# Optimization experiments

Hardware: AMD Instinct MI355X
Metric: run time of the kernel (lower is better)

Reference implementation:

```python
import jax, jax.numpy as jnp
import numpy as np

K = 16  # hard-coded neighborhood size
EPS = 1e-5


def knn_idx(coor_k, coor_q, k):
    # coor_*: (B, 3, N). Returns idx (B, Nq, k) of k nearest points in coor_k for each query.
    inner = jnp.einsum('bcn,bcm->bnm', coor_q, coor_k)
    sq_q = jnp.sum(coor_q ** 2, axis=1)  # (B, Nq)
    sq_k = jnp.sum(coor_k ** 2, axis=1)  # (B, Nk)
    dist = sq_q[:, :, None] + sq_k[:, None, :] - 2.0 * inner  # (B, Nq, Nk)
    return jax.lax.top_k(-dist, k)[1]


def fps(coor, num_group):
    # furthest point sampling, matching pointnet2 (start at index 0, squared dists).
    B, _, N = coor.shape
    xyz = jnp.transpose(coor, (0, 2, 1))  # (B, N, 3)

    def step(carry, _):
        dist, last = carry
        centroid = jnp.take_along_axis(xyz, last[:, None, None], axis=1)  # (B,1,3)
        d = jnp.sum((xyz - centroid) ** 2, axis=-1)  # (B, N)
        dist = jnp.minimum(dist, d)
        nxt = jnp.argmax(dist, axis=1).astype(jnp.int32)
        return (dist, nxt), last

    init = (jnp.full((B, N), 1e10, dtype=coor.dtype), jnp.zeros((B,), jnp.int32))
    _, idxs = jax.lax.scan(step, init, None, length=num_group)
    return jnp.transpose(idxs, (1, 0))  # (B, num_group)


def gather_points(x, idx):
    # x: (B, C, N), idx: (B, S) -> (B, C, S)
    return jnp.take_along_axis(x, idx[:, None, :], axis=2)


def get_graph_feature(coor_q, x_q, coor_k, x_k):
    # coor: (B,3,N), x: (B,C,N) -> (B, 2C, Nq, K)
    B, C, Nq = x_q.shape
    idx = jax.lax.stop_gradient(knn_idx(coor_k, coor_q, K))  # (B, Nq, K)
    idx_flat = jnp.broadcast_to(idx.reshape(B, 1, Nq * K), (B, C, Nq * K))
    nbr = jnp.take_along_axis(x_k, idx_flat, axis=2).reshape(B, C, Nq, K)
    xq = x_q[..., None]  # (B, C, Nq, 1)
    return jnp.concatenate([nbr - xq, jnp.broadcast_to(xq, nbr.shape)], axis=1)


def group_norm(x, gamma, beta, groups):
    # x: (B, C, N, K); normalize over (C//G, N, K) per sample per group.
    B, C = x.shape[0], x.shape[1]
    xr = x.reshape(B, groups, C // groups, *x.shape[2:])
    red = tuple(range(2, xr.ndim))
    mean = jnp.mean(xr, axis=red, keepdims=True)
    var = jnp.mean((xr - mean) ** 2, axis=red, keepdims=True)
    xn = ((xr - mean) * jax.lax.rsqrt(var + EPS)).reshape(x.shape)
    shp = (1, C) + (1,) * (x.ndim - 2)
    return xn * gamma.reshape(shp) + beta.reshape(shp)


def lrelu(x):
    return jnp.where(x >= 0, x, 0.2 * x)


def edge_layer(f, w, g, b):
    # 1x1 conv (no bias) + GroupNorm(4) + LeakyReLU(0.2)
    f = jnp.einsum('oc,bcnk->bonk', w, f)
    return lrelu(group_norm(f, g, b, 4))


def setup_inputs() -> dict:
    key = jax.random.key(0)
    ks = jax.random.split(key, 16)
    B, N = 32, 2048
    p = {}
    p['x'] = jax.random.normal(ks[0], (B, 3, N), dtype=jnp.float32)
    p['w_in'] = jax.random.normal(ks[1], (8, 3), dtype=jnp.float32) * 0.3
    p['b_in'] = jax.random.normal(ks[2], (8,), dtype=jnp.float32) * 0.1
    dims = [(32, 16), (64, 64), (64, 128), (128, 128)]
    for i, (o, c) in enumerate(dims, start=1):
        kw, kg, kb = jax.random.split(ks[2 + i], 3)
        p[f'w{i}'] = jax.random.normal(kw, (o, c), dtype=jnp.float32) * (1.0 / np.sqrt(c))
        p[f'g{i}'] = 1.0 + 0.1 * jax.random.normal(kg, (o,), dtype=jnp.float32)
        p[f'b{i}'] = 0.1 * jax.random.normal(kb, (o,), dtype=jnp.float32)
    return p


def reference(x, w_in, b_in, w1, g1, b1, w2, g2, b2, w3, g3, b3, w4, g4, b4):
    coor = x
    f = jnp.einsum('oc,bcn->bon', w_in, x) + b_in[None, :, None]  # (B,8,N)

    f = get_graph_feature(coor, f, coor, f)          # (B,16,N,K)
    f = jnp.max(edge_layer(f, w1, g1, b1), axis=-1)  # (B,32,N)

    idx = jax.lax.stop_gradient(fps(coor, 512))
    coor_q, f_q = gather_points(coor, idx), gather_points(f, idx)
    f = get_graph_feature(coor_q, f_q, coor, f)      # (B,64,512,K)
    f = jnp.max(edge_layer(f, w2, g2, b2), axis=-1)  # (B,64,512)
    coor = coor_q

    f = get_graph_feature(coor, f, coor, f)          # (B,128,512,K)
    f = jnp.max(edge_layer(f, w3, g3, b3), axis=-1)  # (B,64,512)

    idx = jax.lax.stop_gradient(fps(coor, 128))
    coor_q, f_q = gather_points(coor, idx), gather_points(f, idx)
    f = get_graph_feature(coor_q, f_q, coor, f)      # (B,128,128,K)
    f = jnp.max(edge_layer(f, w4, g4, b4), axis=-1)  # (B,128,128)
    coor = coor_q
    return coor, f
```

## Files before the change

### kernel.cpp

```cpp
#include <hip/hip_runtime.h>
#include <hip/hip_bf16.h>

#define DEV __device__ __forceinline__
typedef unsigned long long u64;

DEV float bf2f(unsigned short u){ return __uint_as_float(((unsigned)u)<<16); }
DEV unsigned short f2bf(float f){
  unsigned u = __float_as_uint(f);
  u += 0x7fffu + ((u>>16)&1u);
  return (unsigned short)(u>>16);
}

template<int CTRL>
DEV u64 dpp_umax(u64 k){
  int lo = (int)(unsigned)k;
  int hi = (int)(unsigned)(k>>32);
  int plo = __builtin_amdgcn_update_dpp(lo, lo, CTRL, 0xF, 0xF, false);
  int phi = __builtin_amdgcn_update_dpp(hi, hi, CTRL, 0xF, 0xF, false);
  u64 p = ((u64)(unsigned)phi << 32) | (unsigned)plo;
  return (p > k) ? p : k;
}

DEV void ce64(u64 &a, u64 &b){
  u64 lo = (a<b)?a:b;
  u64 hi = (a<b)?b:a;
  a = lo; b = hi;
}
DEV void sort8(u64* x){
  #pragma unroll
  for (int k=2;k<=8;k<<=1){
    #pragma unroll
    for (int j=k>>1;j>0;j>>=1){
      #pragma unroll
      for (int i=0;i<8;++i){
        int l = i^j;
        if (l>i){
          if ((i&k)==0) ce64(x[i],x[l]);
          else          ce64(x[l],x[i]);
        }
      }
    }
  }
}
DEV void bm16(u64* A){
  #pragma unroll
  for (int gap=8;gap>0;gap>>=1){
    #pragma unroll
    for (int i=0;i<16;++i){
      if ((i&gap)==0) ce64(A[i], A[i|gap]);
    }
  }
}
DEV unsigned f2sort(float d){
  unsigned ub = __float_as_uint(d);
  unsigned s  = (unsigned)((int)ub >> 31);
  return ub ^ (s | 0x80000000u);
}

struct PConv {
  const void* s[14];
  float*      d[14];
  int         sz[14];
};

__global__ __launch_bounds__(256) void prep_kernel(
    const void* __restrict__ xraw, int* __restrict__ flagw,
    const void* __restrict__ w_in_raw, const void* __restrict__ b_in_raw,
    PConv p,
    float* __restrict__ xyz0, float* __restrict__ f0, float* __restrict__ stats){
  __shared__ int cnt;
  int t = threadIdx.x;
  if (t==0) cnt = 0;
  __syncthreads();
  {
    const unsigned short* xs = (const unsigned short*)xraw;
    int local = 0;
    for (int i=t; i<4096; i+=256){
      int e = (xs[i]>>7)&0xFF;
      if (e >= 0xC0) local++;
    }
    atomicAdd(&cnt, local);
  }
  __syncthreads();
  bool isf = (cnt > 64);
  int bx = blockIdx.x;
  if (bx==0 && t==0) *flagw = isf ? 1 : 0;
  if (bx < 117){
    int i = bx*256 + t;
    int seg = 0, off = i;
    #pragma unroll
    for (seg=0; seg<14; ++seg){
      if (off < p.sz[seg]) break;
      off -= p.sz[seg];
    }
    if (seg >= 14) return;
    float v = isf ? ((const float*)p.s[seg])[off]
                  : bf2f(((const unsigned short*)p.s[seg])[off]);
    p.d[seg][off] = v;
    return;
  }
  int i = (bx-117)*256 + t;
  if (i < 8192) stats[i] = 0.f;
  int b = i >> 11, n = i & 2047;
  size_t base = (size_t)b*3*2048 + n;
  float X, Y, Z;
  if (isf){
    const float* xf = (const float*)xraw;
    X = xf[base]; Y = xf[base+2048]; Z = xf[base+4096];
  } else {
    const unsigned short* xu = (const unsigned short*)xraw;
    X = bf2f(xu[base]); Y = bf2f(xu[base+2048]); Z = bf2f(xu[base+4096]);
  }
  float* o3 = xyz0 + (size_t)i*3;
  o3[0]=X; o3[1]=Y; o3[2]=Z;
  const float* wf = (const float*)w_in_raw;
  const float* bf = (const float*)b_in_raw;
  const unsigned short* wu = (const unsigned short*)w_in_raw;
  const unsigned short* bu = (const unsigned short*)b_in_raw;
  float* fo = f0 + (size_t)i*8;
  #pragma unroll
  for (int o=0;o<8;++o){
    float w0 = isf ? wf[o*3+0] : bf2f(wu[o*3+0]);
    float w1 = isf ? wf[o*3+1] : bf2f(wu[o*3+1]);
    float w2 = isf ? wf[o*3+2] : bf2f(wu[o*3+2]);
    float bb = isf ? bf[o]     : bf2f(bu[o]);
    fo[o] = w0*X + w1*Y + w2*Z + bb;
  }
}

template<int NK, int QB>
DEV void knn_body(float* smem, const float* __restrict__ qxyz,
                  const float* __restrict__ kxyz, int Nq,
                  int* __restrict__ oidx, int bx, int b){
  float4* kd = (float4*)smem;
  u64* lbuf  = (u64*)smem;
  int t = threadIdx.x;
  for (int i=t; i<NK; i+=256){
    const float* p = kxyz + ((size_t)b*NK + i)*3;
    float X=p[0], Y=p[1], Z=p[2];
    float sk = __fadd_rn(__fadd_rn(__fmul_rn(X,X),__fmul_rn(Y,Y)),__fmul_rn(Z,Z));
    kd[i] = make_float4(X,Y,Z,sk);
  }
  __syncthreads();
  int ql = t>>2, h = t&3;
  int q0 = bx*QB;
  const float* qp = qxyz + ((size_t)b*Nq + q0 + ql)*3;
  float QX=qp[0], QY=qp[1], QZ=qp[2];
  float sq = __fadd_rn(__fadd_rn(__fmul_rn(QX,QX),__fmul_rn(QY,QY)),__fmul_rn(QZ,QZ));
  u64 A[16];
  #pragma unroll
  for (int j=0;j<16;++j) A[j] = ~0ULL;
  #pragma unroll 1
  for (int i=0; i<NK/4; i+=8){
    u64 k8[8];
    #pragma unroll
    for (int u=0;u<8;++u){
      int cidx = 4*(i+u)+h;
      float4 c = kd[cidx];
      float dot = __fadd_rn(__fadd_rn(__fmul_rn(QX,c.x),__fmul_rn(QY,c.y)),__fmul_rn(QZ,c.z));
      float d = __fsub_rn(__fadd_rn(sq, c.w), __fmul_rn(2.0f,dot));
      k8[u] = ((u64)f2sort(d)<<32) | (unsigned)cidx;
    }
    sort8(k8);
    #pragma unroll
    for (int s=0;s<8;++s){
      u64 bb = k8[7-s];
      u64 a  = A[8+s];
      A[8+s] = (bb < a) ? bb : a;
    }
    bm16(A);
  }
  __syncthreads();
  u64* Lq = lbuf + ((size_t)ql*65 + (size_t)h*16);
  #pragma unroll
  for (int j=0;j<16;++j) Lq[j] = A[j];
  __syncthreads();
  if (t < QB){
    const u64* db = lbuf + (size_t)t*65;
    int p0=0,p1=0,p2=0,p3=0;
    u64 e0=db[0], e1=db[16], e2=db[32], e3=db[48];
    int* op = oidx + ((size_t)b*Nq + q0 + t)*16;
    #pragma unroll 1
    for (int j=0;j<16;++j){
      u64 bd = e0; int bh = 0;
      if (e1 < bd){ bd=e1; bh=1; }
      if (e2 < bd){ bd=e2; bh=2; }
      if (e3 < bd){ bd=e3; bh=3; }
      op[j] = (int)(unsigned)bd;
      if      (bh==0){ p0++; e0 = (p0<16)? db[p0]    : ~0ULL; }
      else if (bh==1){ p1++; e1 = (p1<16)? db[16+p1] : ~0ULL; }
      else if (bh==2){ p2++; e2 = (p2<16)? db[32+p2] : ~0ULL; }
      else           { p3++; e3 = (p3<16)? db[48+p3] : ~0ULL; }
    }
  }
  __syncthreads();
}

template<int NP,int G>
DEV void fps_body(float* smem, const float* __restrict__ xyz,
                  int* __restrict__ oidx, float* __restrict__ oxyz, int b){
  constexpr int PPT = NP/256;
  __builtin_amdgcn_s_setprio(3);
  float4* xl4 = (float4*)smem;
  u64* candK = (u64*)(smem + NP*4);
  int* selidx = (int*)(smem + NP*4 + 16);
  int t = threadIdx.x, w = t>>6;
  float px[PPT], py[PPT], pz[PPT], dist[PPT];
  #pragma unroll
  for (int j=0;j<PPT;++j){
    int gi = t + j*256;
    const float* p = xyz + ((size_t)b*NP + gi)*3;
    float X=p[0], Y=p[1], Z=p[2];
    px[j]=X; py[j]=Y; pz[j]=Z; dist[j]=1e10f;
    xl4[gi] = make_float4(X,Y,Z,0.f);
  }
  if (t < 8) candK[t] = 0;
  if (t==0) selidx[0] = 0;
  __syncthreads();
  float4 c0 = xl4[0];
  float cx=c0.x, cy=c0.y, cz=c0.z;
  int Bi = 0;
  for (int g=1; g<G; ++g){
    float bv=-1.f; int bi=0;
    #pragma unroll
    for (int j=0;j<PPT;++j){
      float dx=__fsub_rn(px[j],cx), dy=__fsub_rn(py[j],cy), dz=__fsub_rn(pz[j],cz);
      float d = __fadd_rn(__fadd_rn(__fmul_rn(dx,dx),__fmul_rn(dy,dy)),__fmul_rn(dz,dz));
      float nd = fminf(dist[j], d);
      dist[j] = nd;
      bool cc = (nd > bv);
      bv = cc ? nd : bv;
      bi = cc ? (t + j*256) : bi;
    }
    u64 k = ((u64)(unsigned)g << 54)
          | ((u64)__float_as_uint(bv) << 22)
          | (unsigned)(0x3FFFFFu - bi);
    k = dpp_umax<0x111>(k);
    k = dpp_umax<0x112>(k);
    k = dpp_umax<0x114>(k);
    k = dpp_umax<0x118>(k);
    k = dpp_umax<0x142>(k);
    k = dpp_umax<0x143>(k);
    unsigned klo = (unsigned)__builtin_amdgcn_readlane((int)(unsigned)k, 63);
    unsigned khi = (unsigned)__builtin_amdgcn_readlane((int)(unsigned)(k>>32), 63);
    u64 wkey = ((u64)khi<<32) | klo;
    int par = g & 1;
    volatile u64* slots = candK + par*4;
    if ((t&63)==0) slots[w] = wkey;
    u64 kk = wkey;
    #pragma unroll
    for (int ow=0; ow<4; ++ow){
      if (ow == w) continue;
      u64 kv = slots[ow];
      while ((unsigned)(kv>>54) != (unsigned)g){
        __builtin_amdgcn_s_sleep(1);
        kv = slots[ow];
      }
      kk = (kv > kk) ? kv : kk;
    }
    Bi = (int)(0x3FFFFFu - (unsigned)(kk & 0x3FFFFFu));
    float4 c = xl4[Bi];
    cx = c.x; cy = c.y; cz = c.z;
    if (t==0) selidx[g] = Bi;
  }
  __syncthreads();
  for (int i=t; i<G; i+=256){
    int s = selidx[i];
    float4 c = xl4[s];
    oidx[(size_t)b*G + i] = s;
    float* op = oxyz + ((size_t)b*G + i)*3;
    op[0]=c.x; op[1]=c.y; op[2]=c.z;
  }
}

template<int CF,int COUT,int QB>
DEV void edge_body(float* smem, const float* __restrict__ fk,
                   const int* __restrict__ sel, const int* __restrict__ knn,
                   const float* __restrict__ w, float* __restrict__ mm,
                   float* __restrict__ stats, int Nq, int Nk, int bx, int b){
  constexpr int CIN = 2*CF;
  constexpr int GPQ = COUT/2;
  constexpr int WS  = COUT+1;
  constexpr int ESTR= CF*16+8;
  constexpr int WTB = ((CF*WS+3)&~3);
  static_assert(QB*GPQ == 256, "block mapping");
  float* wtb = smem;
  float* e   = smem + WTB;
  float* fqs = e + QB*ESTR;
  float* sS  = fqs + QB*CF;
  int t = threadIdx.x;
  int q0 = bx*QB;

  if (t<8) sS[t]=0.f;
  for (int i=t; i<QB*CF; i+=256){
    int ql = i/CF, c = i&(CF-1);
    int qi = sel ? sel[b*Nq + q0 + ql] : (q0 + ql);
    fqs[i] = fk[((size_t)b*Nk + qi)*CF + c];
  }
  for (int i=t; i<CF*COUT; i+=256){
    int o = i/CF, c = i&(CF-1);
    wtb[c*WS+o] = w[o*CIN + c];
  }
  if (t < QB*16){
    int ql = t>>4, k = t&15;
    int nid = knn[((size_t)b*Nq + q0 + ql)*16 + k];
    const float4* row = (const float4*)(fk + ((size_t)b*Nk + nid)*CF);
    float* ep = e + ql*ESTR + k;
    #pragma unroll
    for (int c4=0; c4<CF/4; ++c4){
      float4 v = row[c4];
      ep[(c4*4+0)*16]=v.x; ep[(c4*4+1)*16]=v.y; ep[(c4*4+2)*16]=v.z; ep[(c4*4+3)*16]=v.w;
    }
  }
  __syncthreads();

  int ql = t/GPQ, o = t%GPQ;
  const float* eb = e + ql*ESTR;
  const float* fqb = fqs + ql*CF;
  float y0[16], y1[16];
  #pragma unroll
  for (int k=0;k<16;++k){ y0[k]=0.f; y1[k]=0.f; }
  float zA0=0.f, zA1=0.f;
  for (int c=0;c<CF;++c){
    float w0 = wtb[c*WS+o];
    float w1 = wtb[c*WS+o+GPQ];
    float fqc = fqb[c];
    zA0 = fmaf(w0,fqc,zA0); zA1 = fmaf(w1,fqc,zA1);
    const float4* ev4 = (const float4*)(eb + c*16);
    #pragma unroll
    for (int k4=0;k4<4;++k4){
      float4 ev = ev4[k4];
      y0[k4*4+0]=fmaf(w0,ev.x,y0[k4*4+0]); y0[k4*4+1]=fmaf(w0,ev.y,y0[k4*4+1]);
      y0[k4*4+2]=fmaf(w0,ev.z,y0[k4*4+2]); y0[k4*4+3]=fmaf(w0,ev.w,y0[k4*4+3]);
      y1[k4*4+0]=fmaf(w1,ev.x,y1[k4*4+0]); y1[k4*4+1]=fmaf(w1,ev.y,y1[k4*4+1]);
      y1[k4*4+2]=fmaf(w1,ev.z,y1[k4*4+2]); y1[k4*4+3]=fmaf(w1,ev.w,y1[k4*4+3]);
    }
  }
  __syncthreads();
  for (int i=t; i<CF*COUT; i+=256){
    int oo = i/CF, c = i&(CF-1);
    wtb[c*WS+oo] = w[oo*CIN + CF + c];
  }
  __syncthreads();
  float zB0=0.f, zB1=0.f;
  for (int c=0;c<CF;++c){
    float fqc = fqb[c];
    zB0 = fmaf(wtb[c*WS+o],fqc,zB0);
    zB1 = fmaf(wtb[c*WS+o+GPQ],fqc,zB1);
  }
  float z0 = zB0 - zA0, z1 = zB1 - zA1;

  float mx0=-3.4e38f, mn0=3.4e38f, s0=0.f, q0s=0.f;
  float mx1=-3.4e38f, mn1=3.4e38f, s1=0.f, q1s=0.f;
  #pragma unroll
  for (int k=0;k<16;++k){
    float v0 = y0[k]+z0, v1 = y1[k]+z1;
    mx0=fmaxf(mx0,v0); mn0=fminf(mn0,v0); s0+=v0; q0s=fmaf(v0,v0,q0s);
    mx1=fmaxf(mx1,v1); mn1=fminf(mn1,v1); s1+=v1; q1s=fmaf(v1,v1,q1s);
  }
  int g0 = o/(COUT/4);
  atomicAdd(&sS[g0],   s0); atomicAdd(&sS[4+g0],   q0s);
  atomicAdd(&sS[g0+2], s1); atomicAdd(&sS[6+g0],   q1s);
  size_t mi0 = ((size_t)b*Nq + q0 + ql)*COUT + o;
  ((float2*)mm)[mi0]       = make_float2(mx0,mn0);
  ((float2*)mm)[mi0+GPQ]   = make_float2(mx1,mn1);
  __syncthreads();
  if (t<8){
    int g = t>>1, which = t&1;
    float val = which ? sS[4+g] : sS[g];
    atomicAdd(&stats[(((size_t)b*4+g)*8 + (bx&7))*2 + which], val);
  }
}

DEV void coor_body(const float* __restrict__ xyz2, void* __restrict__ outbase,
                   const int* __restrict__ flag, int bx){
  int i = bx*256 + threadIdx.x;
  if (i >= 12288) return;
  int m = i & 127;
  int c = (i>>7) % 3;
  int b = i / 384;
  float v = xyz2[((size_t)b*128+m)*3 + c];
  if (*flag) ((float*)outbase)[i] = v;
  else       ((unsigned short*)outbase)[i] = f2bf(v);
}

__global__ __launch_bounds__(256,4) void fused1_kernel(
    const float* __restrict__ xyz0, int* __restrict__ knnb1,
    int* __restrict__ idx1, float* __restrict__ xyz1){
  __shared__ __align__(16) float smem[8752];
  int bx = blockIdx.x;
  if (bx < 32){
    fps_body<2048,512>(smem, xyz0, idx1, xyz1, bx);
  } else {
    int rid = bx - 32;
    knn_body<2048,64>(smem, xyz0, xyz0, 2048, knnb1, rid & 31, rid >> 5);
  }
}

__global__ __launch_bounds__(256,4) void fused2_kernel(
    const float* __restrict__ xyz0, const float* __restrict__ xyz1,
    const int* __restrict__ knnb1,
    int* __restrict__ knnb2, int* __restrict__ knnb3,
    int* __restrict__ idx2, float* __restrict__ xyz2,
    const float* __restrict__ f0, const float* __restrict__ cw1,
    float* __restrict__ mmb, float* __restrict__ stats1){
  __shared__ __align__(16) float smem[8320];
  int bx = blockIdx.x;
  if (bx < 32){
    fps_body<512,128>(smem, xyz1, idx2, xyz2, bx);
  } else if (bx < 288){
    int rid = bx - 32;
    knn_body<2048,64>(smem, xyz1, xyz0, 512, knnb2, rid & 7, rid >> 3);
  } else if (bx < 544){
    int rid = bx - 288;
    knn_body<512,64>(smem, xyz1, xyz1, 512, knnb3, rid & 7, rid >> 3);
  } else {
    int rid = bx - 544;
    edge_body<8,32,16>(smem, f0, nullptr, knnb1, cw1, mmb, stats1,
                       2048, 2048, rid & 127, rid >> 7);
  }
}

__global__ __launch_bounds__(256,4) void fused3_kernel(
    const float* __restrict__ xyz1, const float* __restrict__ xyz2,
    int* __restrict__ knnb4,
    const float* __restrict__ f1, const int* __restrict__ idx1,
    const int* __restrict__ knnb2, const float* __restrict__ cw2,
    float* __restrict__ mmb, float* __restrict__ stats2,
    void* __restrict__ outbase, const int* __restrict__ flag){
  __shared__ __align__(16) float smem[8320];
  int bx = blockIdx.x;
  if (bx < 64){
    knn_body<512,64>(smem, xyz2, xyz1, 128, knnb4, bx & 1, bx >> 1);
  } else if (bx < 2112){
    int rid = bx - 64;
    edge_body<32,64,8>(smem, f1, idx1, knnb2, cw2, mmb, stats2,
                       512, 2048, rid & 63, rid >> 6);
  } else {
    coor_body(xyz2, outbase, flag, bx - 2112);
  }
}

template<int CF,int COUT,int QB>
__global__ __launch_bounds__(256) void edge_kernel(
    const float* __restrict__ fk, const int* __restrict__ sel,
    const int* __restrict__ knn, const float* __restrict__ w,
    float* __restrict__ mm, float* __restrict__ stats, int Nq, int Nk){
  constexpr int WS  = COUT+1;
  constexpr int ESTR= CF*16+8;
  constexpr int WTB = ((CF*WS+3)&~3);
  constexpr int SM  = WTB + QB*ESTR + QB*CF + 8;
  __shared__ __align__(16) float smem[SM];
  edge_body<CF,COUT,QB>(smem, fk, sel, knn, w, mm, stats, Nq, Nk,
                        blockIdx.x, blockIdx.y);
}

__global__ __launch_bounds__(256) void fin_kernel(
    const float* __restrict__ mm, const float* __restrict__ stats,
    const float* __restrict__ gam, const float* __restrict__ bet,
    float* __restrict__ fo, void* __restrict__ outbase, const int* __restrict__ flag,
    int outoff, int Nq, int COUT, float invcnt, int total){
  for (int i = blockIdx.x*256 + threadIdx.x; i<total; i += gridDim.x*256){
    int o = i % COUT;
    int r = i / COUT;
    int q = r % Nq;
    int b = r / Nq;
    int g = o / (COUT>>2);
    const float* sp = stats + ((size_t)(b*4+g))*16;
    float s=0.f, s2=0.f;
    #pragma unroll
    for (int nb=0;nb<8;++nb){ s += sp[nb*2]; s2 += sp[nb*2+1]; }
    float mean = s*invcnt;
    float var  = fmaxf(s2*invcnt - mean*mean, 0.f);
    float inv  = 1.0f / sqrtf(var + 1e-5f);
    float a  = gam[o] * inv;
    float bb = bet[o] - a*mean;
    const float* mp = mm + (size_t)i*2;
    float xv = (a>=0.f) ? mp[0] : mp[1];
    float v = fmaf(a, xv, bb);
    v = (v>=0.f) ? v : 0.2f*v;
    if (fo) fo[i]=v;
    if (outbase){
      int idx = outoff + ((b*COUT + o)*Nq + q);
      if (*flag) ((float*)outbase)[idx] = v;
      else       ((unsigned short*)outbase)[idx] = f2bf(v);
    }
  }
}

extern "C" void kernel_launch(void* const* d_in, const int* in_sizes, int n_in,
                              void* d_out, int out_size, void* d_ws, size_t ws_size,
                              hipStream_t stream){
  float* W    = (float*)d_ws;
  float* xyz0 = W;
  float* f0   = W + 196608;
  float* f1   = W + 720896;
  float* xyz1 = W + 2818048;
  float* f2   = W + 2867200;
  float* f3   = W + 3915776;
  float* xyz2 = W + 4964352;
  float* stats= W + 4976640;
  int*   flag = (int*)(W + 4984832);
  float* PRM  = W + 4984848;
  int*  idx1  = (int*)(W + 5014640);
  int*  idx2  = (int*)(W + 5031024);
  float* SCR  = W + 5035120;
  int*   knnb = (int*)SCR;
  int*   knnb4= (int*)SCR;
  int*   knnb2= (int*)f3;
  int*   knnb3= (int*)f3 + 262144;
  float* mmb  = SCR + 1048576;

  float* cw_in = PRM;
  float* cb_in = PRM+24;
  float* cw1 = PRM+32;   float* cg1 = PRM+544;   float* cbb1 = PRM+576;
  float* cw2 = PRM+608;  float* cg2 = PRM+4704;  float* cbb2 = PRM+4768;
  float* cw3 = PRM+4832; float* cg3 = PRM+13024; float* cbb3 = PRM+13088;
  float* cw4 = PRM+13152;float* cg4 = PRM+29536; float* cbb4 = PRM+29664;

  PConv pc;
  const int psz[14] = {24,8,512,32,32,4096,64,64,8192,64,64,16384,128,128};
  float* pdst[14] = {cw_in,cb_in,cw1,cg1,cbb1,cw2,cg2,cbb2,cw3,cg3,cbb3,cw4,cg4,cbb4};
  for (int j=0;j<14;++j){ pc.s[j]=d_in[j+1]; pc.d[j]=pdst[j]; pc.sz[j]=psz[j]; }

  prep_kernel<<<373,256,0,stream>>>(d_in[0], flag, d_in[1], d_in[2], pc,
                                    xyz0, f0, stats);

  fused1_kernel<<<1056,256,0,stream>>>(xyz0, knnb, idx1, xyz1);

  fused2_kernel<<<4640,256,0,stream>>>(xyz0, xyz1, knnb, knnb2, knnb3,
                                       idx2, xyz2, f0, cw1, mmb, stats+0);

  fin_kernel<<<1024,256,0,stream>>>(mmb, stats+0, cg1, cbb1, f1, nullptr, flag, 0, 2048, 32, 1.f/262144.f, 2097152);

  fused3_kernel<<<2160,256,0,stream>>>(xyz1, xyz2, knnb4,
                                       f1, idx1, knnb2, cw2, mmb, stats+2048,
                                       d_out, flag);
  fin_kernel<<<1024,256,0,stream>>>(mmb, stats+2048, cg2, cbb2, f2, nullptr, flag, 0, 512, 64, 1.f/131072.f, 1048576);

  edge_kernel<64,64,8><<<dim3(64,32),256,0,stream>>>(f2, nullptr, knnb3, cw3, mmb, stats+4096, 512, 512);
  fin_kernel<<<1024,256,0,stream>>>(mmb, stats+4096, cg3, cbb3, f3, nullptr, flag, 0, 512, 64, 1.f/131072.f, 1048576);

  edge_kernel<64,128,4><<<dim3(32,32),256,0,stream>>>(f3, idx2, knnb4, cw4, mmb, stats+6144, 128, 512);
  fin_kernel<<<1024,256,0,stream>>>(mmb, stats+6144, cg4, cbb4, nullptr, d_out, flag, 12288, 128, 128, 1.f/65536.f, 524288);
}
```

Baseline: 669.6 us.

## Run furthest point sampling in a single wavefront per batch

The FPS body now runs on one 64-lane wavefront instead of four. Each lane walks NP/64 points read from LDS every iteration rather than holding coordinates in registers. This removes the per-iteration cross-wave exchange through LDS slots with spin-waits and generation tags, leaving only a DPP reduction and a readlane. The cost is four times more distance work per lane on the serial critical path, plus LDS reads in the inner loop. An empty asm on an offset keeps the compiler from caching those loads in registers.

```diff
diff --git a/kernel.cpp b/kernel.cpp
--- a/kernel.cpp
+++ b/kernel.cpp
@@ -197,44 +197,42 @@
 }
 
 template<int NP,int G>
-DEV void fps_body(float* smem, const float* __restrict__ xyz,
-                  int* __restrict__ oidx, float* __restrict__ oxyz, int b){
-  constexpr int PPT = NP/256;
+DEV void fps_body_sw(float* smem, const float* __restrict__ xyz,
+                     int* __restrict__ oidx, float* __restrict__ oxyz, int b){
+  constexpr int PPT = NP/64;
   __builtin_amdgcn_s_setprio(3);
   float4* xl4 = (float4*)smem;
-  u64* candK = (u64*)(smem + NP*4);
-  int* selidx = (int*)(smem + NP*4 + 16);
-  int t = threadIdx.x, w = t>>6;
-  float px[PPT], py[PPT], pz[PPT], dist[PPT];
+  int* selidx = (int*)(smem + NP*4);
+  int t = threadIdx.x;
+  float dist[PPT];
   #pragma unroll
   for (int j=0;j<PPT;++j){
-    int gi = t + j*256;
+    int gi = t + j*64;
     const float* p = xyz + ((size_t)b*NP + gi)*3;
-    float X=p[0], Y=p[1], Z=p[2];
-    px[j]=X; py[j]=Y; pz[j]=Z; dist[j]=1e10f;
-    xl4[gi] = make_float4(X,Y,Z,0.f);
-  }
-  if (t < 8) candK[t] = 0;
+    xl4[gi] = make_float4(p[0],p[1],p[2],0.f);
+    dist[j] = 1e10f;
+  }
   if (t==0) selidx[0] = 0;
-  __syncthreads();
   float4 c0 = xl4[0];
   float cx=c0.x, cy=c0.y, cz=c0.z;
   int Bi = 0;
+  int zoff = 0;
   for (int g=1; g<G; ++g){
+    __asm__ volatile("" : "+v"(zoff));
     float bv=-1.f; int bi=0;
     #pragma unroll
     for (int j=0;j<PPT;++j){
-      float dx=__fsub_rn(px[j],cx), dy=__fsub_rn(py[j],cy), dz=__fsub_rn(pz[j],cz);
+      int gi = t + j*64;
+      float4 q = xl4[gi + zoff];
+      float dx=__fsub_rn(q.x,cx), dy=__fsub_rn(q.y,cy), dz=__fsub_rn(q.z,cz);
       float d = __fadd_rn(__fadd_rn(__fmul_rn(dx,dx),__fmul_rn(dy,dy)),__fmul_rn(dz,dz));
       float nd = fminf(dist[j], d);
       dist[j] = nd;
       bool cc = (nd > bv);
       bv = cc ? nd : bv;
-      bi = cc ? (t + j*256) : bi;
-    }
-    u64 k = ((u64)(unsigned)g << 54)
-          | ((u64)__float_as_uint(bv) << 22)
-          | (unsigned)(0x3FFFFFu - bi);
+      bi = cc ? gi : bi;
+    }
+    u64 k = ((u64)__float_as_uint(bv)<<32) | (unsigned)(0xFFFFFFFFu - bi);
     k = dpp_umax<0x111>(k);
     k = dpp_umax<0x112>(k);
     k = dpp_umax<0x114>(k);
@@ -242,29 +240,12 @@
     k = dpp_umax<0x142>(k);
     k = dpp_umax<0x143>(k);
     unsigned klo = (unsigned)__builtin_amdgcn_readlane((int)(unsigned)k, 63);
-    unsigned khi = (unsigned)__builtin_amdgcn_readlane((int)(unsigned)(k>>32), 63);
-    u64 wkey = ((u64)khi<<32) | klo;
-    int par = g & 1;
-    volatile u64* slots = candK + par*4;
-    if ((t&63)==0) slots[w] = wkey;
-    u64 kk = wkey;
-    #pragma unroll
-    for (int ow=0; ow<4; ++ow){
-      if (ow == w) continue;
-      u64 kv = slots[ow];
-      while ((unsigned)(kv>>54) != (unsigned)g){
-        __builtin_amdgcn_s_sleep(1);
-        kv = slots[ow];
-      }
-      kk = (kv > kk) ? kv : kk;
-    }
-    Bi = (int)(0x3FFFFFu - (unsigned)(kk & 0x3FFFFFu));
+    Bi = (int)(0xFFFFFFFFu - klo);
     float4 c = xl4[Bi];
     cx = c.x; cy = c.y; cz = c.z;
     if (t==0) selidx[g] = Bi;
   }
-  __syncthreads();
-  for (int i=t; i<G; i+=256){
+  for (int i=t; i<G; i+=64){
     int s = selidx[i];
     float4 c = xl4[s];
     oidx[(size_t)b*G + i] = s;
@@ -390,7 +371,8 @@
   __shared__ __align__(16) float smem[8752];
   int bx = blockIdx.x;
   if (bx < 32){
-    fps_body<2048,512>(smem, xyz0, idx1, xyz1, bx);
+    if (threadIdx.x >= 64) return;
+    fps_body_sw<2048,512>(smem, xyz0, idx1, xyz1, bx);
   } else {
     int rid = bx - 32;
     knn_body<2048,64>(smem, xyz0, xyz0, 2048, knnb1, rid & 31, rid >> 5);
@@ -407,7 +389,8 @@
   __shared__ __align__(16) float smem[8320];
   int bx = blockIdx.x;
   if (bx < 32){
-    fps_body<512,128>(smem, xyz1, idx2, xyz2, bx);
+    if (threadIdx.x >= 64) return;
+    fps_body_sw<512,128>(smem, xyz1, idx2, xyz2, bx);
   } else if (bx < 288){
     int rid = bx - 32;
     knn_body<2048,64>(smem, xyz1, xyz0, 512, knnb2, rid & 7, rid >> 3);
```

Measured after the change: 1.004 ms. 49.9% more time.
